# Kernel tuning notes

Measured on AMD Instinct MI355X. Metric: run time of the kernel, lower is better.

The kernel has to match this reference:

```python
import jax, jax.numpy as jnp
import numpy as np

MIN_PS = 4
MAX_PS = 16


def _enforce(mb):
    # mb: (L,) bool candidate boundaries (merge_signal < 0.7-quantile)
    # Faithful re-implementation of _enforce_patch_size_constraints:
    # walk boundaries left->right, skip segments < MIN_PS (start not advanced),
    # accept otherwise, and insert ceil(ps/MAX_PS)-1 evenly spaced splits for
    # oversized segments. seq_len-1 is always appended as a candidate.
    L = mb.shape[0]
    pos = jnp.arange(L, dtype=jnp.int32)
    cand = mb | (pos == L - 1)

    def fwd_step(start, inp):
        p, is_c = inp
        ps = p - start
        acc = is_c & (ps >= MIN_PS)
        k = jnp.where(acc, (ps + MAX_PS - 1) // MAX_PS, jnp.int32(1))
        sz = jnp.maximum(jnp.where(acc, ps // k, jnp.int32(1)), 1)
        new_start = jnp.where(acc, p, start)
        return new_start, (acc, start, sz, k)

    _, (acc, seg_start, sz, k) = jax.lax.scan(fwd_step, jnp.int32(0), (pos, cand))

    # Reverse scan: propagate each accepted boundary's (start, split_size, num_splits)
    # back to the interior positions of its segment so splits can be placed in parallel.
    def rev_step(carry, inp):
        a, s, z, kk = inp
        cs, cz, ck, cv = carry
        out = (cs, cz, ck, cv)
        ncarry = (jnp.where(a, s, cs), jnp.where(a, z, cz), jnp.where(a, kk, ck), cv | a)
        return ncarry, out

    init = (jnp.int32(0), jnp.int32(1), jnp.int32(1), jnp.bool_(False))
    _, (fs, fz, fk, fv) = jax.lax.scan(rev_step, init, (acc, seg_start, sz, k), reverse=True)
    r = pos - fs
    j = r // fz
    split = fv & (r > 0) & (r % fz == 0) & (j >= 1) & (j <= fk - 1)
    return acc | split


def reference(x, attention_mask, W1, b1, W2, b2, Wc, bc, Wb1, bb1, Wb2, bb2):
    B, L, D = x.shape
    # content scorer: Linear -> ReLU -> Linear -> Sigmoid
    content = jax.nn.sigmoid(jax.nn.relu(x @ W1 + b1) @ W2 + b2)[..., 0]  # (B, L)
    # grouped Conv1d(d, d//2, k=3, pad=1, groups=d//4)
    xc = jnp.transpose(x, (0, 2, 1))  # (B, D, L)
    pf = jax.lax.conv_general_dilated(xc, Wc, (1,), ((1, 1),),
                                      feature_group_count=D // 4,
                                      dimension_numbers=('NCH', 'OIH', 'NCH'))
    pf = jnp.transpose(pf + bc[None, :, None], (0, 2, 1))  # (B, L, D//2)
    comb = jnp.concatenate([x, pf], axis=-1)
    bscore = jax.nn.sigmoid(jax.nn.relu(comb @ Wb1 + bb1) @ Wb2 + bb2)[..., 0]  # (B, L)
    signal = content * (1.0 - bscore) * attention_mask
    thr = jnp.quantile(signal, 0.7, axis=1, keepdims=True)
    mb = signal < thr
    new_b = jax.vmap(_enforce)(mb)  # (B, L) bool, new_b[:,0] is always False

    # segment id per token = inclusive cumsum of boundaries
    seg = jnp.cumsum(new_b.astype(jnp.int32), axis=1)
    seg_flat = (seg + jnp.arange(B, dtype=jnp.int32)[:, None] * L).reshape(-1)
    NS = B * L
    xm = x * attention_mask[..., None]
    e = jnp.sum(xm * xm, axis=-1).reshape(-1)  # softmax logits = ||token||^2
    m = jax.ops.segment_max(e, seg_flat, num_segments=NS)
    w = jnp.exp(e - m[seg_flat])
    denom = jax.ops.segment_sum(w, seg_flat, num_segments=NS)
    wn = w / denom[seg_flat]
    merged = jax.ops.segment_sum(xm.reshape(-1, D) * wn[:, None], seg_flat,
                                 num_segments=NS).reshape(B, L, D)
    # segment_boundaries: 1 for every segment except the first, zero padding
    n_last = seg[:, -1]
    p = jnp.arange(L)
    seg_bounds = ((p[None, :] >= 1) & (p[None, :] <= n_last[:, None])).astype(jnp.float32)
    return merged, seg_bounds


def setup_inputs() -> dict:
    key = jax.random.key(0)
    B, L, D = 4, 8192, 512
    ks = jax.random.split(key, 8)
    s = 0.02
    return {
        'x': jax.random.normal(ks[0], (B, L, D), jnp.float32),
        'attention_mask': jnp.ones((B, L), jnp.float32),
        'W1': jax.random.normal(ks[1], (D, D // 4), jnp.float32) * s,
        'b1': jnp.zeros((D // 4,), jnp.float32),
        'W2': jax.random.normal(ks[2], (D // 4, 1), jnp.float32) * s,
        'b2': jnp.zeros((1,), jnp.float32),
        'Wc': jax.random.normal(ks[3], (D // 2, 4, 3), jnp.float32) * s,
        'bc': jnp.zeros((D // 2,), jnp.float32),
        'Wb1': jax.random.normal(ks[4], (D + D // 2, D // 4), jnp.float32) * s,
        'bb1': jnp.zeros((D // 4,), jnp.float32),
        'Wb2': jax.random.normal(ks[5], (D // 4, 1), jnp.float32) * s,
        'bb2': jnp.zeros((1,), jnp.float32),
    }
```

## Files before the change

### kernel.cpp

```cpp
#include <hip/hip_runtime.h>
#include <math.h>

#define B_  4
#define L_  8192
#define D_  512
#define BL_ (B_*L_)
#define TOK 64
#define XS  68
#define KC  16
#define NCH (D_/KC)

__global__ __launch_bounds__(256, 2) void k_signal(
    const float* __restrict__ x, const float* __restrict__ mask,
    const float* __restrict__ W1, const float* __restrict__ b1,
    const float* __restrict__ W2, const float* __restrict__ b2,
    const float* __restrict__ Wc, const float* __restrict__ bc,
    const float* __restrict__ Wb1, const float* __restrict__ bb1,
    const float* __restrict__ Wb2, const float* __restrict__ bb2,
    float* __restrict__ signal, float* __restrict__ e,
    unsigned int* __restrict__ hist,
    float* __restrict__ merged, float* __restrict__ bounds)
{
  __shared__ float ws1[KC][128];
  __shared__ float wsb[KC][128];
  __shared__ float wsp[8][128];
  __shared__ float xt[KC][XS];
  __shared__ float pf[8][XS];

  const int t   = threadIdx.x;
  const int blk = blockIdx.x;
  const int b   = blk >> 7;
  const int l0  = (blk & 127) << 6;
  const float* xb = x + (size_t)b * L_ * D_;

  const int jq = t & 31, tw = t >> 5;
  const int j0 = jq << 2, tok0 = tw << 3;

  const int stok = t >> 2, skk = t & 3;
  const int oo_c = t >> 5;
  const int m2   = (t & 31) << 1;
  const int cb_c = (oo_c >> 1) << 2;

  const int srow = t >> 5, sc4 = (t & 31) << 2;

  if (t < 16) {
    float4* bz = reinterpret_cast<float4*>(bounds + (size_t)b * L_ + l0);
    bz[t] = make_float4(0.f, 0.f, 0.f, 0.f);
  }
  float4* mz = reinterpret_cast<float4*>(merged + (size_t)(b * L_ + l0) * D_);

  float a1[8][4], a2[8][4];
#pragma unroll
  for (int i = 0; i < 8; ++i)
#pragma unroll
    for (int j = 0; j < 4; ++j) { a1[i][j] = 0.f; a2[i][j] = 0.f; }
  float esacc = 0.f;

  float4 r_w1a, r_w1b, r_wba, r_wbb, r_wp, r_xv, r_hv;
  float4 r_wc0, r_wc1, r_wc2;
  float  r_bc;

  auto LOAD = [&](int c) {
    const int kc = c << 4;
    r_w1a = *reinterpret_cast<const float4*>(W1  + (size_t)(kc + srow) * 128 + sc4);
    r_w1b = *reinterpret_cast<const float4*>(W1  + (size_t)(kc + 8 + srow) * 128 + sc4);
    r_wba = *reinterpret_cast<const float4*>(Wb1 + (size_t)(kc + srow) * 128 + sc4);
    r_wbb = *reinterpret_cast<const float4*>(Wb1 + (size_t)(kc + 8 + srow) * 128 + sc4);
    r_wp  = *reinterpret_cast<const float4*>(Wb1 + (size_t)(512 + (c << 3) + srow) * 128 + sc4);
    r_xv  = *reinterpret_cast<const float4*>(xb + (size_t)(l0 + stok) * D_ + kc + (skk << 2));
    if (t < 8) {
      const int hh = t >> 2, kk = t & 3;
      const int l = hh ? (l0 + TOK) : (l0 - 1);
      r_hv = make_float4(0.f, 0.f, 0.f, 0.f);
      if (l >= 0 && l < L_)
        r_hv = *reinterpret_cast<const float4*>(xb + (size_t)l * D_ + kc + (kk << 2));
    }
    const int o = (c << 3) + oo_c;
    const float* wcp = Wc + o * 12;
    r_wc0 = *reinterpret_cast<const float4*>(wcp);
    r_wc1 = *reinterpret_cast<const float4*>(wcp + 4);
    r_wc2 = *reinterpret_cast<const float4*>(wcp + 8);
    r_bc  = bc[o];
  };

  LOAD(0);

  for (int c = 0; c < NCH; ++c) {
    __syncthreads();

    *reinterpret_cast<float4*>(&ws1[srow][sc4])     = r_w1a;
    *reinterpret_cast<float4*>(&ws1[8 + srow][sc4]) = r_w1b;
    *reinterpret_cast<float4*>(&wsb[srow][sc4])     = r_wba;
    *reinterpret_cast<float4*>(&wsb[8 + srow][sc4]) = r_wbb;
    *reinterpret_cast<float4*>(&wsp[srow][sc4])     = r_wp;
    {
      const float4 v = r_xv;
      esacc = fmaf(v.x, v.x, esacc); esacc = fmaf(v.y, v.y, esacc);
      esacc = fmaf(v.z, v.z, esacc); esacc = fmaf(v.w, v.w, esacc);
      const int r = skk << 2;
      xt[r + 0][stok] = v.x; xt[r + 1][stok] = v.y;
      xt[r + 2][stok] = v.z; xt[r + 3][stok] = v.w;
    }
    if (t < 8) {
      const int hh = t >> 2, kk = t & 3;
      const int col = TOK + hh, r = kk << 2;
      xt[r + 0][col] = r_hv.x; xt[r + 1][col] = r_hv.y;
      xt[r + 2][col] = r_hv.z; xt[r + 3][col] = r_hv.w;
    }
    __syncthreads();

    float wcl[12];
    wcl[0] = r_wc0.x; wcl[1]  = r_wc0.y; wcl[2]  = r_wc0.z; wcl[3]  = r_wc0.w;
    wcl[4] = r_wc1.x; wcl[5]  = r_wc1.y; wcl[6]  = r_wc1.z; wcl[7]  = r_wc1.w;
    wcl[8] = r_wc2.x; wcl[9]  = r_wc2.y; wcl[10] = r_wc2.z; wcl[11] = r_wc2.w;
    const float bcv = r_bc;

    if (c + 1 < NCH) LOAD(c + 1);

    mz[(c << 8) + t] = make_float4(0.f, 0.f, 0.f, 0.f);

    {
      float pa = bcv, pb = bcv;
      const int tm1 = (m2 == 0) ? TOK : m2 - 1;
      const int tp2 = (m2 + 2 == TOK) ? TOK + 1 : m2 + 2;
#pragma unroll
      for (int i = 0; i < 4; ++i) {
        const float* row = &xt[cb_c + i][0];
        const float  xm1 = row[tm1];
        const float2 x01 = *reinterpret_cast<const float2*>(&row[m2]);
        const float  xp2 = row[tp2];
        pa = fmaf(xm1,   wcl[i * 3 + 0], pa);
        pa = fmaf(x01.x, wcl[i * 3 + 1], pa);
        pa = fmaf(x01.y, wcl[i * 3 + 2], pa);
        pb = fmaf(x01.x, wcl[i * 3 + 0], pb);
        pb = fmaf(x01.y, wcl[i * 3 + 1], pb);
        pb = fmaf(xp2,   wcl[i * 3 + 2], pb);
      }
      *reinterpret_cast<float2*>(&pf[oo_c][m2]) = make_float2(pa, pb);
    }

#pragma unroll 4
    for (int k = 0; k < KC; ++k) {
      const float4 w1 = *reinterpret_cast<const float4*>(&ws1[k][j0]);
      const float4 wb = *reinterpret_cast<const float4*>(&wsb[k][j0]);
      const float4 xa = *reinterpret_cast<const float4*>(&xt[k][tok0]);
      const float4 xc = *reinterpret_cast<const float4*>(&xt[k][tok0 + 4]);
      const float xs8[8] = {xa.x, xa.y, xa.z, xa.w, xc.x, xc.y, xc.z, xc.w};
#pragma unroll
      for (int i = 0; i < 8; ++i) {
        a1[i][0] = fmaf(xs8[i], w1.x, a1[i][0]);
        a1[i][1] = fmaf(xs8[i], w1.y, a1[i][1]);
        a1[i][2] = fmaf(xs8[i], w1.z, a1[i][2]);
        a1[i][3] = fmaf(xs8[i], w1.w, a1[i][3]);
        a2[i][0] = fmaf(xs8[i], wb.x, a2[i][0]);
        a2[i][1] = fmaf(xs8[i], wb.y, a2[i][1]);
        a2[i][2] = fmaf(xs8[i], wb.z, a2[i][2]);
        a2[i][3] = fmaf(xs8[i], wb.w, a2[i][3]);
      }
    }
    __syncthreads();

#pragma unroll 2
    for (int oo = 0; oo < 8; ++oo) {
      const float4 wp = *reinterpret_cast<const float4*>(&wsp[oo][j0]);
      const float4 pa4 = *reinterpret_cast<const float4*>(&pf[oo][tok0]);
      const float4 pb4 = *reinterpret_cast<const float4*>(&pf[oo][tok0 + 4]);
      const float ps8[8] = {pa4.x, pa4.y, pa4.z, pa4.w, pb4.x, pb4.y, pb4.z, pb4.w};
#pragma unroll
      for (int i = 0; i < 8; ++i) {
        a2[i][0] = fmaf(ps8[i], wp.x, a2[i][0]);
        a2[i][1] = fmaf(ps8[i], wp.y, a2[i][1]);
        a2[i][2] = fmaf(ps8[i], wp.z, a2[i][2]);
        a2[i][3] = fmaf(ps8[i], wp.w, a2[i][3]);
      }
    }
  }

  float sigv[8];
#pragma unroll
  for (int i = 0; i < 8; ++i) sigv[i] = 0.f;
  {
    float b1v[4], w2v[4], bbv[4], wv2[4];
#pragma unroll
    for (int jj = 0; jj < 4; ++jj) {
      b1v[jj] = b1[j0 + jj];  w2v[jj] = W2[j0 + jj];
      bbv[jj] = bb1[j0 + jj]; wv2[jj] = Wb2[j0 + jj];
    }
    const float bias2 = b2[0], biasb2 = bb2[0];
#pragma unroll
    for (int i = 0; i < 8; ++i) {
      float p1 = 0.f, p2 = 0.f;
#pragma unroll
      for (int jj = 0; jj < 4; ++jj) {
        const float h1 = a1[i][jj] + b1v[jj];
        if (h1 > 0.f) p1 = fmaf(h1, w2v[jj], p1);
        const float h2 = a2[i][jj] + bbv[jj];
        if (h2 > 0.f) p2 = fmaf(h2, wv2[jj], p2);
      }
#pragma unroll
      for (int off = 1; off < 32; off <<= 1) {
        p1 += __shfl_xor(p1, off, 64);
        p2 += __shfl_xor(p2, off, 64);
      }
      if (jq == 0) {
        const int gi = b * L_ + l0 + tok0 + i;
        const float content = 1.f / (1.f + expf(-(p1 + bias2)));
        const float bscore  = 1.f / (1.f + expf(-(p2 + biasb2)));
        const float s = content * (1.f - bscore) * mask[gi];
        sigv[i] = s;
        signal[gi] = s;
      }
    }
  }

  {
    float es = esacc;
    es += __shfl_xor(es, 1, 64);
    es += __shfl_xor(es, 2, 64);
    if (skk == 0) {
      const int gi = b * L_ + l0 + stok;
      const float m = mask[gi];
      e[gi] = m * m * es;
    }
  }

  {
    __syncthreads();
    unsigned int* hl = reinterpret_cast<unsigned int*>(&xt[0][0]);
    hl[t & 255] = 0u;
    __syncthreads();
    if (jq == 0) {
#pragma unroll
      for (int i = 0; i < 8; ++i) {
        const unsigned int u = __float_as_uint(sigv[i]);
        const unsigned int key = (u & 0x80000000u) ? ~u : (u | 0x80000000u);
        atomicAdd(&hl[key >> 24], 1u);
      }
    }
    __syncthreads();
    const unsigned int cnt = hl[t & 255];
    if (cnt) atomicAdd(&hist[(b << 8) + (t & 255)], cnt);
  }
}

__device__ __forceinline__ int chain_sim(unsigned long long w, int from) {
  int last = -1;
  while (from < 64) {
    const unsigned long long m = w & (~0ull << from);
    if (m == 0ull) break;
    const int p = __ffsll(m) - 1;
    last = p;
    from = p + 4;
  }
  return last;
}

__global__ __launch_bounds__(1024) void k_select(
    const float* __restrict__ signal, const unsigned int* __restrict__ hist,
    int* __restrict__ starts, int* __restrict__ nlast)
{
  __shared__ unsigned int bins[4][256];
  __shared__ unsigned int sel_prefix;
  __shared__ int sel_rank;
  __shared__ float sh_thr;
  __shared__ unsigned int wmin[16];
  __shared__ int wcnt[16];
  __shared__ unsigned long long cw[128];
  __shared__ unsigned char nb[L_];
  __shared__ signed char tbl[128][4];
  __shared__ int st_in[128];
  __shared__ int offs[257];

  const int b = blockIdx.x, t = threadIdx.x;
  const int wv = t >> 6, lane = t & 63;
  const float* s = signal + b * L_;

  float val[8];
  unsigned int key[8];
#pragma unroll
  for (int i = 0; i < 8; ++i) {
    val[i] = s[(i << 10) + t];
    const unsigned int u = __float_as_uint(val[i]);
    key[i] = (u & 0x80000000u) ? ~u : (u | 0x80000000u);
  }

  if (t < 256) bins[0][t] = hist[(b << 8) + t];
  __syncthreads();
  if (t < 64) {
    const unsigned int c0 = bins[0][(t << 2) + 0], c1 = bins[0][(t << 2) + 1];
    const unsigned int c2 = bins[0][(t << 2) + 2], c3 = bins[0][(t << 2) + 3];
    const unsigned int lsum = c0 + c1 + c2 + c3;
    unsigned int run = lsum;
#pragma unroll
    for (int off = 1; off < 64; off <<= 1) {
      const unsigned int v = __shfl_up(run, off, 64);
      if (t >= off) run += v;
    }
    const int r = 5733;
    if (r >= (int)(run - lsum) && r < (int)run) {
      int rr = r - (int)(run - lsum);
      unsigned int cbin;
      if (rr < (int)c0) { cbin = 0; }
      else if (rr < (int)(c0 + c1)) { cbin = 1; rr -= (int)c0; }
      else if (rr < (int)(c0 + c1 + c2)) { cbin = 2; rr -= (int)(c0 + c1); }
      else { cbin = 3; rr -= (int)(c0 + c1 + c2); }
      sel_rank = rr;
      sel_prefix = (unsigned int)(t << 2) | cbin;
    }
  }
  __syncthreads();

  for (int round = 1; round < 4; ++round) {
    reinterpret_cast<unsigned int*>(bins)[t] = 0u;
    __syncthreads();
    const unsigned int pre = sel_prefix;
    const int shift = 24 - 8 * round;
#pragma unroll
    for (int i = 0; i < 8; ++i) {
      if ((key[i] >> (shift + 8)) == pre)
        atomicAdd(&bins[t >> 8][(key[i] >> shift) & 255u], 1u);
    }
    __syncthreads();
    if (t < 256)
      bins[0][t] = bins[0][t] + bins[1][t] + bins[2][t] + bins[3][t];
    __syncthreads();
    if (t < 64) {
      const unsigned int c0 = bins[0][(t << 2) + 0], c1 = bins[0][(t << 2) + 1];
      const unsigned int c2 = bins[0][(t << 2) + 2], c3 = bins[0][(t << 2) + 3];
      const unsigned int lsum = c0 + c1 + c2 + c3;
      unsigned int run = lsum;
#pragma unroll
      for (int off = 1; off < 64; off <<= 1) {
        const unsigned int v = __shfl_up(run, off, 64);
        if (t >= off) run += v;
      }
      const int r = sel_rank;
      if (r >= (int)(run - lsum) && r < (int)run) {
        int rr = r - (int)(run - lsum);
        unsigned int cbin;
        if (rr < (int)c0) { cbin = 0; }
        else if (rr < (int)(c0 + c1)) { cbin = 1; rr -= (int)c0; }
        else if (rr < (int)(c0 + c1 + c2)) { cbin = 2; rr -= (int)(c0 + c1); }
        else { cbin = 3; rr -= (int)(c0 + c1 + c2); }
        sel_rank = rr;
        sel_prefix = (pre << 8) | ((unsigned int)(t << 2) | cbin);
      }
    }
    __syncthreads();
  }
  const unsigned int k0 = sel_prefix;

  {
    int cle = 0;
    unsigned int mgt = 0xFFFFFFFFu;
#pragma unroll
    for (int i = 0; i < 8; ++i) {
      if (key[i] <= k0) ++cle;
      else mgt = min(mgt, key[i]);
    }
#pragma unroll
    for (int off = 1; off < 64; off <<= 1) {
      cle += __shfl_xor(cle, off, 64);
      mgt = min(mgt, (unsigned int)__shfl_xor((int)mgt, off, 64));
    }
    if (lane == 0) { wcnt[wv] = cle; wmin[wv] = mgt; }
    __syncthreads();
    if (t == 0) {
      int C = 0; unsigned int M = 0xFFFFFFFFu;
      for (int g = 0; g < 16; ++g) { C += wcnt[g]; M = min(M, wmin[g]); }
      const unsigned int k1 = (C >= 5735) ? k0 : M;
      const unsigned int u0 = (k0 & 0x80000000u) ? (k0 & 0x7fffffffu) : ~k0;
      const unsigned int u1 = (k1 & 0x80000000u) ? (k1 & 0x7fffffffu) : ~k1;
      const float v0 = __uint_as_float(u0);
      const float v1 = __uint_as_float(u1);
      const float g = 0.7f * 8191.0f - 5733.0f;
      sh_thr = v0 + g * (v1 - v0);
    }
    __syncthreads();
  }
  const float thr = sh_thr;

#pragma unroll
  for (int i = 0; i < 8; ++i) {
    const unsigned long long m = __ballot(val[i] < thr);
    if (lane == 0) cw[(i << 4) + wv] = m;
  }
  {
    const int base = t << 3;
#pragma unroll
    for (int i = 0; i < 8; ++i) nb[base + i] = 0;
  }
  __syncthreads();
  if (t == 0) cw[127] |= (1ull << 63);
  __syncthreads();

  if (t < 512) {
    const int blk = t >> 2, cls = t & 3;
    tbl[blk][cls] = (signed char)chain_sim(cw[blk], cls);
  }
  __syncthreads();

  if (t == 0) {
    int st = 0;
    for (int blk = 0; blk < 128; ++blk) {
      const int bs = blk << 6;
      st_in[blk] = st;
      int pl;
      if (blk == 0) {
        pl = chain_sim(cw[0], 4);
      } else {
        int off = st + 4 - bs;
        if (off < 0) off = 0;
        pl = tbl[blk][off];
      }
      if (pl >= 0) st = bs + pl;
    }
  }
  __syncthreads();

  if (t < 128) {
    const int bs = t << 6;
    const unsigned long long w = cw[t];
    int st = st_in[t];
    int from = st + 4 - bs;
    if (from < 0) from = 0;
    while (from < 64) {
      const unsigned long long m = w & (~0ull << from);
      if (m == 0ull) break;
      const int p_rel = __ffsll(m) - 1;
      const int p = bs + p_rel;
      nb[p] = 1;
      const int ps = p - st;
      const int k = (ps + 15) >> 4;
      if (k > 1) {
        int sz = ps / k; if (sz < 1) sz = 1;
        for (int j = 1; j < k; ++j) nb[st + j * sz] = 1;
      }
      st = p;
      from = p_rel + 4;
    }
  }
  __syncthreads();

  int ls = 0, run = 0;
  if (t < 256) {
    const int base = t << 5;
    for (int i = 0; i < 32; ++i) ls += nb[base + i];
    run = ls;
#pragma unroll
    for (int off = 1; off < 64; off <<= 1) {
      const int v = __shfl_up(run, off, 64);
      if ((t & 63) >= off) run += v;
    }
    if ((t & 63) == 63) wcnt[t >> 6] = run;
  }
  __syncthreads();
  if (t < 256) {
    const int w = t >> 6;
    int addb = 0;
    if (w > 0) addb += wcnt[0];
    if (w > 1) addb += wcnt[1];
    if (w > 2) addb += wcnt[2];
    offs[t] = addb + run - ls;
    if (t == 255) offs[256] = addb + run;
  }
  __syncthreads();
  if (t < 256) {
    const int base = t << 5;
    int rn = offs[t];
    for (int i = 0; i < 32; ++i) {
      rn += nb[base + i];
      if (nb[base + i]) starts[b * L_ + rn] = base + i;
    }
  }
  if (t == 0) { starts[b * L_ + 0] = 0; nlast[b] = offs[256]; }
}

__global__ __launch_bounds__(256) void k_merge(const float* __restrict__ x,
    const float* __restrict__ mask, const float* __restrict__ e,
    const int* __restrict__ starts, const int* __restrict__ nlast,
    float* __restrict__ merged, float* __restrict__ bounds)
{
  const int idx = (blockIdx.x << 2) + (threadIdx.x >> 6);
  const int b   = idx >> 13;
  const int sid = idx & (L_ - 1);
  const int n = nlast[b];
  if (sid > n) return;
  const int lane = threadIdx.x & 63;
  if (lane == 0 && sid >= 1)
    bounds[(size_t)b * L_ + sid] = 1.0f;
  const int c0 = lane << 3;
  float* o = merged + (size_t)(b * L_ + sid) * D_ + c0;
  const int t0 = starts[b * L_ + sid];
  const int t1 = (sid < n) ? starts[b * L_ + sid + 1] : L_;
  const int len = t1 - t0;
  const float* eb = e + b * L_;

  float acc[8] = {0,0,0,0,0,0,0,0};

  if (len <= 64) {
    const float ev = (lane < len) ? eb[t0 + lane] : -INFINITY;
    float mx = ev;
#pragma unroll
    for (int off = 1; off < 64; off <<= 1)
      mx = fmaxf(mx, __shfl_xor(mx, off, 64));
    const float ex = expf(ev - mx);
    float den = ex;
#pragma unroll
    for (int off = 1; off < 64; off <<= 1)
      den += __shfl_xor(den, off, 64);
    const float mk = (lane < len) ? mask[b * L_ + t0 + lane] : 0.f;
    const float scl = (ex / den) * mk;

    const float* xr = x + (size_t)(b * L_ + t0) * D_ + c0;
    float4 u0 = reinterpret_cast<const float4*>(xr)[0];
    float4 u1 = reinterpret_cast<const float4*>(xr)[1];
    for (int r = 0; r < len; ++r) {
      float4 n0, n1;
      if (r + 1 < len) {
        const float* xn = xr + (size_t)(r + 1) * D_;
        n0 = reinterpret_cast<const float4*>(xn)[0];
        n1 = reinterpret_cast<const float4*>(xn)[1];
      }
      const float sc = __shfl(scl, r, 64);
      acc[0] = fmaf(sc, u0.x, acc[0]); acc[1] = fmaf(sc, u0.y, acc[1]);
      acc[2] = fmaf(sc, u0.z, acc[2]); acc[3] = fmaf(sc, u0.w, acc[3]);
      acc[4] = fmaf(sc, u1.x, acc[4]); acc[5] = fmaf(sc, u1.y, acc[5]);
      acc[6] = fmaf(sc, u1.z, acc[6]); acc[7] = fmaf(sc, u1.w, acc[7]);
      u0 = n0; u1 = n1;
    }
  } else {
    float mx = -INFINITY;
    for (int p = t0; p < t1; ++p) mx = fmaxf(mx, eb[p]);
    float den = 0.f;
    for (int p = t0; p < t1; ++p) den += expf(eb[p] - mx);
    for (int p = t0; p < t1; ++p) {
      const float wn = expf(eb[p] - mx) / den;
      const float sc = wn * mask[b * L_ + p];
      const float* xr = x + ((size_t)(b * L_ + p)) * D_ + c0;
      const float4 u0 = reinterpret_cast<const float4*>(xr)[0];
      const float4 u1 = reinterpret_cast<const float4*>(xr)[1];
      acc[0] = fmaf(sc, u0.x, acc[0]); acc[1] = fmaf(sc, u0.y, acc[1]);
      acc[2] = fmaf(sc, u0.z, acc[2]); acc[3] = fmaf(sc, u0.w, acc[3]);
      acc[4] = fmaf(sc, u1.x, acc[4]); acc[5] = fmaf(sc, u1.y, acc[5]);
      acc[6] = fmaf(sc, u1.z, acc[6]); acc[7] = fmaf(sc, u1.w, acc[7]);
    }
  }
  reinterpret_cast<float4*>(o)[0] = make_float4(acc[0], acc[1], acc[2], acc[3]);
  reinterpret_cast<float4*>(o)[1] = make_float4(acc[4], acc[5], acc[6], acc[7]);
}

extern "C" void kernel_launch(void* const* d_in, const int* in_sizes, int n_in,
                              void* d_out, int out_size, void* d_ws, size_t ws_size,
                              hipStream_t stream) {
  (void)in_sizes; (void)n_in; (void)out_size; (void)ws_size;
  const float* x    = (const float*)d_in[0];
  const float* mask = (const float*)d_in[1];
  const float* W1   = (const float*)d_in[2];
  const float* b1   = (const float*)d_in[3];
  const float* W2   = (const float*)d_in[4];
  const float* b2   = (const float*)d_in[5];
  const float* Wc   = (const float*)d_in[6];
  const float* bc   = (const float*)d_in[7];
  const float* Wb1  = (const float*)d_in[8];
  const float* bb1  = (const float*)d_in[9];
  const float* Wb2  = (const float*)d_in[10];
  const float* bb2  = (const float*)d_in[11];

  float* merged = (float*)d_out;
  float* bounds = (float*)d_out + (size_t)BL_ * D_;

  char* ws = (char*)d_ws;
  float*        signal = (float*)(ws);
  float*        e      = (float*)(ws + (size_t)BL_ * 4);
  int*          starts = (int*)  (ws + (size_t)BL_ * 8);
  int*          nlast  = (int*)  (ws + (size_t)BL_ * 12);
  unsigned int* hist   = (unsigned int*)(ws + (size_t)BL_ * 12 + 256);

  hipMemsetAsync(hist, 0, B_ * 256 * sizeof(unsigned int), stream);
  k_signal<<<BL_ / TOK, 256, 0, stream>>>(x, mask, W1, b1, W2, b2, Wc, bc,
                                          Wb1, bb1, Wb2, bb2, signal, e,
                                          hist, merged, bounds);
  k_select<<<B_, 1024, 0, stream>>>(signal, hist, starts, nlast);
  k_merge<<<BL_ / 4, 256, 0, stream>>>(x, mask, e, starts, nlast, merged, bounds);
}
```

Measured before the change: 299.8 us.

## Build 16-bit radix histogram in signal kernel to skip a select round

The signal kernel now builds a 65536-bin per-batch histogram over the top 16 key bits using global atomics, replacing the 8-bit shared-memory histogram. The select kernel finds the quantile bin with a two-level scan over that histogram and starts its refinement rounds at round 2, removing one full pass over the keys. The cost is a larger memset (1 MB), scattered global atomics per token, and a 64-load-per-thread scan in the single-block select kernel.

```diff
diff --git a/kernel.cpp b/kernel.cpp
--- a/kernel.cpp
+++ b/kernel.cpp
@@ -18,7 +18,7 @@
     const float* __restrict__ Wb1, const float* __restrict__ bb1,
     const float* __restrict__ Wb2, const float* __restrict__ bb2,
     float* __restrict__ signal, float* __restrict__ e,
-    unsigned int* __restrict__ hist,
+    unsigned int* __restrict__ hist16,
     float* __restrict__ merged, float* __restrict__ bounds)
 {
   __shared__ float ws1[KC][128];
@@ -176,9 +176,6 @@
     }
   }
 
-  float sigv[8];
-#pragma unroll
-  for (int i = 0; i < 8; ++i) sigv[i] = 0.f;
   {
     float b1v[4], w2v[4], bbv[4], wv2[4];
 #pragma unroll
@@ -207,8 +204,11 @@
         const float content = 1.f / (1.f + expf(-(p1 + bias2)));
         const float bscore  = 1.f / (1.f + expf(-(p2 + biasb2)));
         const float s = content * (1.f - bscore) * mask[gi];
-        sigv[i] = s;
         signal[gi] = s;
+        const unsigned int u = __float_as_uint(s);
+        const unsigned int key = (u & 0x80000000u) ? ~u : (u | 0x80000000u);
+        const unsigned int bb16 = key >> 16;
+        atomicAdd(&hist16[((unsigned)b << 16) | ((bb16 & 63u) << 10) | (bb16 >> 6)], 1u);
       }
     }
   }
@@ -223,24 +223,6 @@
       e[gi] = m * m * es;
     }
   }
-
-  {
-    __syncthreads();
-    unsigned int* hl = reinterpret_cast<unsigned int*>(&xt[0][0]);
-    hl[t & 255] = 0u;
-    __syncthreads();
-    if (jq == 0) {
-#pragma unroll
-      for (int i = 0; i < 8; ++i) {
-        const unsigned int u = __float_as_uint(sigv[i]);
-        const unsigned int key = (u & 0x80000000u) ? ~u : (u | 0x80000000u);
-        atomicAdd(&hl[key >> 24], 1u);
-      }
-    }
-    __syncthreads();
-    const unsigned int cnt = hl[t & 255];
-    if (cnt) atomicAdd(&hist[(b << 8) + (t & 255)], cnt);
-  }
 }
 
 __device__ __forceinline__ int chain_sim(unsigned long long w, int from) {
@@ -256,12 +238,14 @@
 }
 
 __global__ __launch_bounds__(1024) void k_select(
-    const float* __restrict__ signal, const unsigned int* __restrict__ hist,
+    const float* __restrict__ signal, const unsigned int* __restrict__ hist16,
     int* __restrict__ starts, int* __restrict__ nlast)
 {
   __shared__ unsigned int bins[4][256];
   __shared__ unsigned int sel_prefix;
   __shared__ int sel_rank;
+  __shared__ int sel_tt, sel_rr;
+  __shared__ unsigned int wpart[16];
   __shared__ float sh_thr;
   __shared__ unsigned int wmin[16];
   __shared__ int wcnt[16];
@@ -274,6 +258,7 @@
   const int b = blockIdx.x, t = threadIdx.x;
   const int wv = t >> 6, lane = t & 63;
   const float* s = signal + b * L_;
+  const unsigned int* hb = hist16 + ((unsigned)b << 16);
 
   float val[8];
   unsigned int key[8];
@@ -284,33 +269,44 @@
     key[i] = (u & 0x80000000u) ? ~u : (u | 0x80000000u);
   }
 
-  if (t < 256) bins[0][t] = hist[(b << 8) + t];
-  __syncthreads();
-  if (t < 64) {
-    const unsigned int c0 = bins[0][(t << 2) + 0], c1 = bins[0][(t << 2) + 1];
-    const unsigned int c2 = bins[0][(t << 2) + 2], c3 = bins[0][(t << 2) + 3];
-    const unsigned int lsum = c0 + c1 + c2 + c3;
-    unsigned int run = lsum;
+  unsigned int tsum = 0;
+#pragma unroll 8
+  for (int i = 0; i < 64; ++i) tsum += hb[(i << 10) | t];
+  {
+    unsigned int run = tsum;
 #pragma unroll
     for (int off = 1; off < 64; off <<= 1) {
       const unsigned int v = __shfl_up(run, off, 64);
-      if (t >= off) run += v;
-    }
+      if (lane >= off) run += v;
+    }
+    if (lane == 63) wpart[wv] = run;
+    __syncthreads();
+    unsigned int wadd = 0;
+    for (int g = 0; g < wv; ++g) wadd += wpart[g];
+    run += wadd;
+    const unsigned int excl = run - tsum;
     const int r = 5733;
-    if (r >= (int)(run - lsum) && r < (int)run) {
-      int rr = r - (int)(run - lsum);
-      unsigned int cbin;
-      if (rr < (int)c0) { cbin = 0; }
-      else if (rr < (int)(c0 + c1)) { cbin = 1; rr -= (int)c0; }
-      else if (rr < (int)(c0 + c1 + c2)) { cbin = 2; rr -= (int)(c0 + c1); }
-      else { cbin = 3; rr -= (int)(c0 + c1 + c2); }
-      sel_rank = rr;
-      sel_prefix = (unsigned int)(t << 2) | cbin;
-    }
-  }
-  __syncthreads();
-
-  for (int round = 1; round < 4; ++round) {
+    if (r >= (int)excl && r < (int)run) { sel_tt = t; sel_rr = r - (int)excl; }
+    __syncthreads();
+    if (t < 64) {
+      const int tt = sel_tt, rr = sel_rr;
+      const unsigned int cnt = hb[(t << 10) | tt];
+      unsigned int irun = cnt;
+#pragma unroll
+      for (int off = 1; off < 64; off <<= 1) {
+        const unsigned int v = __shfl_up(irun, off, 64);
+        if (t >= off) irun += v;
+      }
+      const unsigned int iexcl = irun - cnt;
+      if (rr >= (int)iexcl && rr < (int)irun) {
+        sel_prefix = ((unsigned int)tt << 6) | (unsigned int)t;
+        sel_rank   = rr - (int)iexcl;
+      }
+    }
+    __syncthreads();
+  }
+
+  for (int round = 2; round < 4; ++round) {
     reinterpret_cast<unsigned int*>(bins)[t] = 0u;
     __syncthreads();
     const unsigned int pre = sel_prefix;
@@ -442,17 +438,17 @@
   }
   __syncthreads();
 
-  int ls = 0, run = 0;
+  int ls = 0, run2 = 0;
   if (t < 256) {
     const int base = t << 5;
     for (int i = 0; i < 32; ++i) ls += nb[base + i];
-    run = ls;
+    run2 = ls;
 #pragma unroll
     for (int off = 1; off < 64; off <<= 1) {
-      const int v = __shfl_up(run, off, 64);
-      if ((t & 63) >= off) run += v;
-    }
-    if ((t & 63) == 63) wcnt[t >> 6] = run;
+      const int v = __shfl_up(run2, off, 64);
+      if ((t & 63) >= off) run2 += v;
+    }
+    if ((t & 63) == 63) wcnt[t >> 6] = run2;
   }
   __syncthreads();
   if (t < 256) {
@@ -461,8 +457,8 @@
     if (w > 0) addb += wcnt[0];
     if (w > 1) addb += wcnt[1];
     if (w > 2) addb += wcnt[2];
-    offs[t] = addb + run - ls;
-    if (t == 255) offs[256] = addb + run;
+    offs[t] = addb + run2 - ls;
+    if (t == 255) offs[256] = addb + run2;
   }
   __syncthreads();
   if (t < 256) {
@@ -575,12 +571,12 @@
   float*        e      = (float*)(ws + (size_t)BL_ * 4);
   int*          starts = (int*)  (ws + (size_t)BL_ * 8);
   int*          nlast  = (int*)  (ws + (size_t)BL_ * 12);
-  unsigned int* hist   = (unsigned int*)(ws + (size_t)BL_ * 12 + 256);
-
-  hipMemsetAsync(hist, 0, B_ * 256 * sizeof(unsigned int), stream);
+  unsigned int* hist16 = (unsigned int*)(ws + (size_t)BL_ * 12 + 1024);
+
+  hipMemsetAsync(hist16, 0, (size_t)B_ * 65536 * sizeof(unsigned int), stream);
   k_signal<<<BL_ / TOK, 256, 0, stream>>>(x, mask, W1, b1, W2, b2, Wc, bc,
                                           Wb1, bb1, Wb2, bb2, signal, e,
-                                          hist, merged, bounds);
-  k_select<<<B_, 1024, 0, stream>>>(signal, hist, starts, nlast);
+                                          hist16, merged, bounds);
+  k_select<<<B_, 1024, 0, stream>>>(signal, hist16, starts, nlast);
   k_merge<<<BL_ / 4, 256, 0, stream>>>(x, mask, e, starts, nlast, merged, bounds);
 }
```

After: 292.1 us. 2.6% less time.
